# Kernel tuning notes

Measured on AMD Instinct MI355X. Metric: run time of the kernel, lower is better.

## Reference

```python
import jax, jax.numpy as jnp
import numpy as np

DIM = 1024
N_HEADS = 16
HEAD_DIM = DIM // N_HEADS
SCALE = HEAD_DIM ** (-0.5)


def setup_inputs() -> dict:
    key = jax.random.key(0)
    ks = jax.random.split(key, 5)
    B, N = 2, 1024
    x = jax.random.normal(ks[0], (B, N, DIM), dtype=jnp.float32)
    # torch nn.Linear convention: weight is (out_features, in_features)
    w_qkvg = jax.random.normal(ks[1], (4 * DIM, DIM), dtype=jnp.float32) * (DIM ** -0.5)
    b_qkvg = jax.random.normal(ks[2], (4 * DIM,), dtype=jnp.float32) * 0.02
    w_proj = jax.random.normal(ks[3], (DIM, DIM), dtype=jnp.float32) * (DIM ** -0.5)
    b_proj = jax.random.normal(ks[4], (DIM,), dtype=jnp.float32) * 0.02
    return {"x": x, "w_qkvg": w_qkvg, "b_qkvg": b_qkvg, "w_proj": w_proj, "b_proj": b_proj}


def reference(x, w_qkvg, b_qkvg, w_proj, b_proj):
    B, N, dim = x.shape
    # fused qkvg projection: (B, N, 4*dim)
    qkvg = x @ w_qkvg.T + b_qkvg
    # (B, N, 4, H, hd) -> (4, B, H, N, hd)
    qkvg = qkvg.reshape(B, N, 4, N_HEADS, HEAD_DIM).transpose(2, 0, 3, 1, 4)
    q = jax.nn.softplus(qkvg[0])          # (B, H, N, hd)
    k = jax.nn.softplus(qkvg[1])          # (B, H, N, hd)
    v = jax.nn.gelu(qkvg[2], approximate=False)  # (B, H, N, hd)
    g = jax.nn.gelu(qkvg[3], approximate=False)  # (B, H, N, hd)
    # kv = k @ v^T over head_dim -> (B, H, N, N)
    kv = jnp.einsum('bhnd,bhmd->bhnm', k, v)
    # z: contract q over tokens with per-token k-sums -> (B, H, hd)
    z = jnp.einsum('bhcn,bhc->bhn', q, k.sum(axis=-1)) * SCALE
    z = 1.0 / (z + dim)
    # out[b,h,d,n] = sum_c q[b,h,c,n] * kv[b,h,c,d] -> (B, H, N, hd)
    out = jnp.einsum('bhcn,bhcd->bhdn', q, kv) * SCALE
    out = (out + v) * z[:, :, None, :]    # broadcast z over token axis
    out = out.reshape(B, N, dim)          # raw reshape, faithful to original
    out = out * g.reshape(B, N, dim)
    out = out @ w_proj.T + b_proj
    return out
```

## Files before the change

kernel.cpp:

```cpp
#include <hip/hip_runtime.h>
#include <hip/hip_bf16.h>
#include <math.h>

typedef float f32x4 __attribute__((ext_vector_type(4)));
typedef __bf16 bf16_t;
typedef bf16_t bf16x8 __attribute__((ext_vector_type(8)));
typedef bf16_t bf16x4 __attribute__((ext_vector_type(4)));

__device__ __forceinline__ float act_softplus(float x) {
    return fmaxf(x, 0.f) + log1pf(expf(-fabsf(x)));
}
__device__ __forceinline__ float act_gelu(float x) {
    return 0.5f * x * (1.f + erff(x * 0.70710678118654752f));
}

__device__ __forceinline__ void gload_lds16(const bf16_t* g, bf16_t* l) {
    __builtin_amdgcn_global_load_lds(
        (const __attribute__((address_space(1))) unsigned int*)g,
        (__attribute__((address_space(3))) unsigned int*)l, 16, 0, 0);
}

template<int N_IMM>
__device__ __forceinline__ void wait_vmcnt() {
    if constexpr (N_IMM == 0) asm volatile("s_waitcnt vmcnt(0)" ::: "memory");
    else if constexpr (N_IMM == 2) asm volatile("s_waitcnt vmcnt(2)" ::: "memory");
    else if constexpr (N_IMM == 4) asm volatile("s_waitcnt vmcnt(4)" ::: "memory");
    else static_assert(N_IMM == 0, "unsupported vmcnt");
}

__global__ __launch_bounds__(256) void cvt3(const float* __restrict__ a, bf16_t* __restrict__ ao, int na4,
                                            const float* __restrict__ b, bf16_t* __restrict__ bo, int nb4,
                                            const float* __restrict__ c, bf16_t* __restrict__ co, int nc4) {
    int q = blockIdx.x * 256 + threadIdx.x;
    const float* src; bf16_t* dst;
    if (q < na4)            { src = a + (size_t)q * 4;              dst = ao + (size_t)q * 4; }
    else if (q < na4 + nb4) { int r = q - na4; src = b + (size_t)r * 4; dst = bo + (size_t)r * 4; }
    else if (q < na4 + nb4 + nc4) { int r = q - na4 - nb4; src = c + (size_t)r * 4; dst = co + (size_t)r * 4; }
    else return;
    float4 v = *reinterpret_cast<const float4*>(src);
    bf16x4 o;
    o[0] = (bf16_t)v.x; o[1] = (bf16_t)v.y; o[2] = (bf16_t)v.z; o[3] = (bf16_t)v.w;
    *reinterpret_cast<bf16x4*>(dst) = o;
}

__global__ __launch_bounds__(256) void gemm_qkvg(const bf16_t* __restrict__ A,
                                                 const bf16_t* __restrict__ Wall,
                                                 const float* __restrict__ biasAll,
                                                 bf16_t* __restrict__ OutAll) {
    constexpr int BM = 64, BN = 64, MR = 2, NR = 2;
    constexpr int K = 1024, M = 2048, N = 1024;
    constexpr int TNUM = K / 32;
    constexpr int LOADS = 2;

    __shared__ __align__(16) bf16_t Sa0[BM * 32];
    __shared__ __align__(16) bf16_t Sb0[BN * 32];
    __shared__ __align__(16) bf16_t Sa1[BM * 32];
    __shared__ __align__(16) bf16_t Sb1[BN * 32];

    const int sec = blockIdx.x >> 9;
    const int bid = blockIdx.x & 511;
    const bf16_t* B = Wall + (size_t)sec * 1024 * 1024;
    const float* bias = biasAll + sec * 1024;
    bf16_t* Cout = OutAll + (size_t)sec * 2048 * 1024;

    const int tid = threadIdx.x;
    const int lane = tid & 63;
    const int w = tid >> 6;
    const int wr = w >> 1, wc = w & 1;

    const int NTM = M / BM, NTN = N / BN;
    const int CHM = NTM >> 3;
    const int chunkN = (NTN * CHM) >> 3;
    const int c = bid & 7;
    const int pp = bid >> 3;
    const int mt = (c % CHM) * 8 + (pp & 7);
    const int nt = (c / CHM) * chunkN + (pp >> 3);
    const int m0 = mt * BM, n0 = nt * BN;

    const int l15 = lane & 15, lg = lane >> 4;
    const int srow = lane >> 2, pos = lane & 3;

    f32x4 acc[MR][NR] = {};

    auto stageTo = [&](bf16_t* Ad, bf16_t* Bd, int k0) {
        int row = w * 16 + srow;
        int ch = pos ^ ((row >> 1) & 3);
        gload_lds16(&A[(size_t)(m0 + row) * K + k0 + ch * 8], &Ad[w * 512]);
        gload_lds16(&B[(size_t)(n0 + row) * K + k0 + ch * 8], &Bd[w * 512]);
    };

    auto compute = [&](const bf16_t* Ac, const bf16_t* Bc) {
        bf16x8 af[MR], bfr[NR];
#pragma unroll
        for (int i = 0; i < MR; ++i) {
            int ar = wr * MR * 16 + i * 16 + l15;
            af[i] = *(const bf16x8*)(&Ac[ar * 32 + (lg ^ ((ar >> 1) & 3)) * 8]);
        }
#pragma unroll
        for (int j = 0; j < NR; ++j) {
            int br = wc * NR * 16 + j * 16 + l15;
            bfr[j] = *(const bf16x8*)(&Bc[br * 32 + (lg ^ ((br >> 1) & 3)) * 8]);
        }
#pragma unroll
        for (int i = 0; i < MR; ++i)
#pragma unroll
            for (int j = 0; j < NR; ++j)
                acc[i][j] = __builtin_amdgcn_mfma_f32_16x16x32_bf16(af[i], bfr[j], acc[i][j], 0, 0, 0);
    };

    stageTo(Sa0, Sb0, 0);
    for (int t = 0; t < TNUM; t += 2) {
        if (t + 1 < TNUM) { stageTo(Sa1, Sb1, (t + 1) * 32); wait_vmcnt<LOADS>(); }
        else              { wait_vmcnt<0>(); }
        __builtin_amdgcn_s_barrier();
        __builtin_amdgcn_sched_barrier(0);
        compute(Sa0, Sb0);
        __builtin_amdgcn_sched_barrier(0);
        __builtin_amdgcn_s_barrier();

        if (t + 2 < TNUM) { stageTo(Sa0, Sb0, (t + 2) * 32); wait_vmcnt<LOADS>(); }
        else              { wait_vmcnt<0>(); }
        __builtin_amdgcn_s_barrier();
        __builtin_amdgcn_sched_barrier(0);
        compute(Sa1, Sb1);
        __builtin_amdgcn_sched_barrier(0);
        __builtin_amdgcn_s_barrier();
    }

    bf16_t* slab = &Sb1[w * 512];
#pragma unroll
    for (int i = 0; i < MR; ++i) {
#pragma unroll
        for (int j = 0; j < NR; ++j) {
            int gn = n0 + wc * 32 + j * 16 + l15;
            float bv = bias[gn];
#pragma unroll
            for (int r = 0; r < 4; ++r) {
                float v = acc[i][j][r] + bv;
                float a = (sec < 2) ? act_softplus(v) : act_gelu(v);
                slab[(lg * 4 + r) * 32 + j * 16 + l15] = (bf16_t)a;
            }
        }
        int row = lane >> 2, c8 = (lane & 3) * 8;
        bf16x8 val = *(const bf16x8*)(&slab[row * 32 + c8]);
        *(bf16x8*)(&Cout[(size_t)(m0 + wr * 32 + i * 16 + row) * N + n0 + wc * 32 + c8]) = val;
        __builtin_amdgcn_s_barrier();
    }
}

template<int BM, int BN, int MR, int NR>
__global__ __launch_bounds__(256) void gemm_bt(const bf16_t* __restrict__ A,
                                               const bf16_t* __restrict__ B,
                                               const float* __restrict__ bias,
                                               float* __restrict__ Cout,
                                               int M, int N) {
    constexpr int K = 1024;
    constexpr int TNUM = K / 32;
    constexpr int WCOLS = BN / (NR * 16);
    constexpr int WROWS = BM / (MR * 16);
    static_assert(WROWS * WCOLS == 4, "4 waves");
    constexpr int ASEG = BM / 64, BSEG = BN / 64;
    constexpr int LOADS = ASEG + BSEG;

    __shared__ __align__(16) bf16_t Sa0[BM * 32];
    __shared__ __align__(16) bf16_t Sb0[BN * 32];
    __shared__ __align__(16) bf16_t Sa1[BM * 32];
    __shared__ __align__(16) bf16_t Sb1[BN * 32];
    __shared__ __align__(16) bf16_t Sa2[BM * 32];
    __shared__ __align__(16) bf16_t Sb2[BN * 32];

    const int tid = threadIdx.x;
    const int lane = tid & 63;
    const int w = tid >> 6;
    const int wr = w / WCOLS, wc = w % WCOLS;

    const int NTM = M / BM, NTN = N / BN;
    const int CHM = NTM >> 3;
    const int chunkN = (NTN * CHM) >> 3;
    const int c = blockIdx.x & 7;
    const int pp = blockIdx.x >> 3;
    const int mt = (c % CHM) * 8 + (pp & 7);
    const int nt = (c / CHM) * chunkN + (pp >> 3);
    const int m0 = mt * BM, n0 = nt * BN;

    const int l15 = lane & 15, lg = lane >> 4;
    const int srow = lane >> 2, pos = lane & 3;

    f32x4 acc[MR][NR] = {};

    auto stageTo = [&](bf16_t* Ad, bf16_t* Bd, int k0) {
#pragma unroll
        for (int t = 0; t < ASEG; ++t) {
            int s = w + t * 4;
            int row = s * 16 + srow;
            int ch = pos ^ ((row >> 1) & 3);
            gload_lds16(&A[(size_t)(m0 + row) * K + k0 + ch * 8], &Ad[s * 512]);
        }
#pragma unroll
        for (int t = 0; t < BSEG; ++t) {
            int s = w + t * 4;
            int row = s * 16 + srow;
            int ch = pos ^ ((row >> 1) & 3);
            gload_lds16(&B[(size_t)(n0 + row) * K + k0 + ch * 8], &Bd[s * 512]);
        }
    };

    auto compute = [&](const bf16_t* Ac, const bf16_t* Bc) {
        bf16x8 af[MR], bfr[NR];
#pragma unroll
        for (int i = 0; i < MR; ++i) {
            int ar = wr * MR * 16 + i * 16 + l15;
            af[i] = *(const bf16x8*)(&Ac[ar * 32 + (lg ^ ((ar >> 1) & 3)) * 8]);
        }
#pragma unroll
        for (int j = 0; j < NR; ++j) {
            int br = wc * NR * 16 + j * 16 + l15;
            bfr[j] = *(const bf16x8*)(&Bc[br * 32 + (lg ^ ((br >> 1) & 3)) * 8]);
        }
#pragma unroll
        for (int i = 0; i < MR; ++i)
#pragma unroll
            for (int j = 0; j < NR; ++j)
                acc[i][j] = __builtin_amdgcn_mfma_f32_16x16x32_bf16(af[i], bfr[j], acc[i][j], 0, 0, 0);
    };

    stageTo(Sa0, Sb0, 0);
    stageTo(Sa1, Sb1, 32);

    for (int t = 0; t < TNUM - 2; t += 3) {
        wait_vmcnt<LOADS>();
        __builtin_amdgcn_s_barrier();
        __builtin_amdgcn_sched_barrier(0);
        stageTo(Sa2, Sb2, (t + 2) * 32);
        compute(Sa0, Sb0);
        __builtin_amdgcn_sched_barrier(0);

        wait_vmcnt<LOADS>();
        __builtin_amdgcn_s_barrier();
        __builtin_amdgcn_sched_barrier(0);
        stageTo(Sa0, Sb0, (t + 3) * 32);
        compute(Sa1, Sb1);
        __builtin_amdgcn_sched_barrier(0);

        wait_vmcnt<LOADS>();
        __builtin_amdgcn_s_barrier();
        __builtin_amdgcn_sched_barrier(0);
        stageTo(Sa1, Sb1, (t + 4) * 32);
        compute(Sa2, Sb2);
        __builtin_amdgcn_sched_barrier(0);
    }
    wait_vmcnt<LOADS>();
    __builtin_amdgcn_s_barrier();
    __builtin_amdgcn_sched_barrier(0);
    compute(Sa0, Sb0);
    __builtin_amdgcn_sched_barrier(0);

    wait_vmcnt<0>();
    __builtin_amdgcn_s_barrier();
    __builtin_amdgcn_sched_barrier(0);
    compute(Sa1, Sb1);

#pragma unroll
    for (int i = 0; i < MR; ++i) {
        int gm_base = m0 + wr * MR * 16 + i * 16 + lg * 4;
#pragma unroll
        for (int j = 0; j < NR; ++j) {
            int gn = n0 + wc * NR * 16 + j * 16 + l15;
            float bv = bias[gn];
#pragma unroll
            for (int r = 0; r < 4; ++r) {
                int gm = gm_base + r;
                Cout[(size_t)gm * N + gn] = acc[i][j][r] + bv;
            }
        }
    }
}

__global__ __launch_bounds__(256) void attn_A(const bf16_t* __restrict__ qkvga,
                                              float* __restrict__ Apart) {
    const int bh = blockIdx.x;
    const int p = blockIdx.y;
    const int b = bh >> 4, h = bh & 15;
    const int tid = threadIdx.x;
    __shared__ float ks[32][64];
    __shared__ float qs[32][64];
    float acc[4][4] = {};
    const int dg = tid >> 4, eg = tid & 15;
    const int stok = tid >> 3, se0 = (tid & 7) * 8;
    const bf16_t* qf = qkvga;
    const bf16_t* kf = qkvga + (size_t)2048 * 1024;

    for (int t0 = p * 128; t0 < p * 128 + 128; t0 += 32) {
        __syncthreads();
        size_t rowb = (size_t)(b * 1024 + t0 + stok) * 1024 + h * 64 + se0;
        bf16x8 qv8 = *(const bf16x8*)(&qf[rowb]);
        bf16x8 kv8 = *(const bf16x8*)(&kf[rowb]);
#pragma unroll
        for (int jj = 0; jj < 8; ++jj) {
            qs[stok][se0 + jj] = (float)qv8[jj];
            ks[stok][se0 + jj] = (float)kv8[jj];
        }
        __syncthreads();
#pragma unroll 8
        for (int tt = 0; tt < 32; ++tt) {
            f32x4 kv = *(const f32x4*)(&ks[tt][dg * 4]);
            f32x4 qv = *(const f32x4*)(&qs[tt][eg * 4]);
#pragma unroll
            for (int i = 0; i < 4; ++i)
#pragma unroll
                for (int j = 0; j < 4; ++j) acc[i][j] += kv[i] * qv[j];
        }
    }
    float* dst = Apart + ((size_t)p * 32 + bh) * 4096;
#pragma unroll
    for (int i = 0; i < 4; ++i)
#pragma unroll
        for (int j = 0; j < 4; ++j)
            dst[(dg * 4 + i) * 64 + eg * 4 + j] = acc[i][j];
}

__global__ __launch_bounds__(256) void reduce_A_z(const float* __restrict__ Apart,
                                                  float* __restrict__ A,
                                                  float* __restrict__ z) {
    const int bh = blockIdx.x;
    const int tid = threadIdx.x;
    __shared__ float As[4096];
    for (int i0 = tid * 4; i0 < 4096; i0 += 1024) {
        f32x4 s = {};
#pragma unroll
        for (int p = 0; p < 8; ++p) {
            f32x4 v = *(const f32x4*)(&Apart[((size_t)p * 32 + bh) * 4096 + i0]);
            s += v;
        }
        *(f32x4*)(&As[i0]) = s;
        *(f32x4*)(&A[(size_t)bh * 4096 + i0]) = s;
    }
    __syncthreads();
    if (tid < 64) {
        float s = 0.f;
#pragma unroll 8
        for (int d = 0; d < 64; ++d) s += As[d * 64 + tid];
        z[bh * 64 + tid] = 1.0f / (s * 0.125f + 1024.0f);
    }
}

__global__ __launch_bounds__(256) void out_Y(const bf16_t* __restrict__ qkvga,
                                             const float* __restrict__ A,
                                             const float* __restrict__ z,
                                             bf16_t* __restrict__ Y) {
    const int bh = blockIdx.x;
    const int b = bh >> 4, h = bh & 15;
    const int chunk = blockIdx.y;
    const int tid = threadIdx.x;
    __shared__ float As[64][64];
    __shared__ float vs[32][64];
    __shared__ float zs[64];
    for (int i = tid; i < 4096; i += 256) As[i >> 6][i & 63] = A[(size_t)bh * 4096 + i];
    if (tid < 64) zs[tid] = z[bh * 64 + tid];
    const bf16_t* vf = qkvga + (size_t)2 * 2048 * 1024;
    const bf16_t* gf = qkvga + (size_t)3 * 2048 * 1024;
    const int e = tid & 63, trow = tid >> 6;
    const int stok = tid >> 3, se0 = (tid & 7) * 8;

    for (int t0 = chunk * 64; t0 < chunk * 64 + 64; t0 += 32) {
        __syncthreads();
        bf16x8 vv8 = *(const bf16x8*)(&vf[(size_t)(b * 1024 + t0 + stok) * 1024 + h * 64 + se0]);
#pragma unroll
        for (int jj = 0; jj < 8; ++jj) vs[stok][se0 + jj] = (float)vv8[jj];
        __syncthreads();
#pragma unroll
        for (int kk = 0; kk < 8; ++kk) {
            int ml = trow * 8 + kk;
            int m = t0 + ml;
            float s = 0.f;
#pragma unroll 8
            for (int d = 0; d < 64; ++d) s += vs[ml][d] * As[d][e];
            float g = (float)gf[(size_t)(b * 1024 + m) * 1024 + h * 64 + e];
            float o = (s * 0.125f + vs[ml][e]) * zs[e] * g;
            Y[((size_t)b * 1024 + h * 64 + (m >> 4)) * 1024 + ((m & 15) << 6) + e] = (bf16_t)o;
        }
    }
}

extern "C" void kernel_launch(void* const* d_in, const int* in_sizes, int n_in,
                              void* d_out, int out_size, void* d_ws, size_t ws_size,
                              hipStream_t stream) {
    const float* x      = (const float*)d_in[0];
    const float* w_qkvg = (const float*)d_in[1];
    const float* b_qkvg = (const float*)d_in[2];
    const float* w_proj = (const float*)d_in[3];
    const float* b_proj = (const float*)d_in[4];

    char* p = (char*)d_ws;
    bf16_t* xb    = (bf16_t*)p; p += (size_t)2048 * 1024 * 2;
    bf16_t* w1b   = (bf16_t*)p; p += (size_t)4096 * 1024 * 2;
    bf16_t* w2b   = (bf16_t*)p; p += (size_t)1024 * 1024 * 2;
    bf16_t* qkvga = (bf16_t*)p; p += (size_t)4 * 2048 * 1024 * 2;
    float*  Apart = (float*)p;  p += (size_t)8 * 32 * 4096 * 4;
    float*  Afull = (float*)p;  p += (size_t)32 * 4096 * 4;
    float*  zbuf  = (float*)p;  p += (size_t)32 * 64 * 4;
    bf16_t* Ybuf  = (bf16_t*)p; p += (size_t)2048 * 1024 * 2;

    cvt3<<<7168, 256, 0, stream>>>(x, xb, 524288, w_qkvg, w1b, 1048576, w_proj, w2b, 262144);

    gemm_qkvg<<<2048, 256, 0, stream>>>(xb, w1b, b_qkvg, qkvga);

    attn_A<<<dim3(32, 8), 256, 0, stream>>>(qkvga, Apart);
    reduce_A_z<<<32, 256, 0, stream>>>(Apart, Afull, zbuf);
    out_Y<<<dim3(32, 16), 256, 0, stream>>>(qkvga, Afull, zbuf, Ybuf);
    gemm_bt<64, 64, 2, 2><<<512, 256, 0, stream>>>(Ybuf, w2b, b_proj, (float*)d_out, 2048, 1024);
}
```

Baseline: 95.79 us.

## Rewrite QKVG projection GEMM with 256x256 tiles, 8 waves and triple buffering

```diff
diff --git a/kernel.cpp b/kernel.cpp
--- a/kernel.cpp
+++ b/kernel.cpp
@@ -43,108 +43,133 @@
     *reinterpret_cast<bf16x4*>(dst) = o;
 }
 
-__global__ __launch_bounds__(256) void gemm_qkvg(const bf16_t* __restrict__ A,
+__global__ __launch_bounds__(512) void gemm1_8ph(const bf16_t* __restrict__ Ag,
                                                  const bf16_t* __restrict__ Wall,
                                                  const float* __restrict__ biasAll,
                                                  bf16_t* __restrict__ OutAll) {
-    constexpr int BM = 64, BN = 64, MR = 2, NR = 2;
-    constexpr int K = 1024, M = 2048, N = 1024;
-    constexpr int TNUM = K / 32;
-    constexpr int LOADS = 2;
-
-    __shared__ __align__(16) bf16_t Sa0[BM * 32];
-    __shared__ __align__(16) bf16_t Sb0[BN * 32];
-    __shared__ __align__(16) bf16_t Sa1[BM * 32];
-    __shared__ __align__(16) bf16_t Sb1[BN * 32];
-
-    const int sec = blockIdx.x >> 9;
-    const int bid = blockIdx.x & 511;
-    const bf16_t* B = Wall + (size_t)sec * 1024 * 1024;
-    const float* bias = biasAll + sec * 1024;
-    bf16_t* Cout = OutAll + (size_t)sec * 2048 * 1024;
+    constexpr int K = 1024;
+    constexpr int NKT = K / 32;
+    __shared__ __align__(16) bf16_t SA0[256 * 32];
+    __shared__ __align__(16) bf16_t SA1[256 * 32];
+    __shared__ __align__(16) bf16_t SA2[256 * 32];
+    __shared__ __align__(16) bf16_t SB0[256 * 32];
+    __shared__ __align__(16) bf16_t SB1[256 * 32];
+    __shared__ __align__(16) bf16_t SB2[256 * 32];
 
     const int tid = threadIdx.x;
     const int lane = tid & 63;
     const int w = tid >> 6;
-    const int wr = w >> 1, wc = w & 1;
-
-    const int NTM = M / BM, NTN = N / BN;
-    const int CHM = NTM >> 3;
-    const int chunkN = (NTN * CHM) >> 3;
-    const int c = bid & 7;
-    const int pp = bid >> 3;
-    const int mt = (c % CHM) * 8 + (pp & 7);
-    const int nt = (c / CHM) * chunkN + (pp >> 3);
-    const int m0 = mt * BM, n0 = nt * BN;
+    const int wr = w >> 2, wc = w & 3;
+
+    const int c = blockIdx.x & 7;
+    const int pp = blockIdx.x >> 3;
+    const int mt = pp & 7;
+    const int nt = c * 2 + (pp >> 3);
+    const int m0 = mt * 256;
+    const int sec = nt >> 2;
+    const int nc0 = (nt & 3) * 256;
+    const bf16_t* Bg = Wall + (size_t)sec * 1024 * 1024;
+    const float* bias = biasAll + sec * 1024;
+    bf16_t* Cout = OutAll + (size_t)sec * 2048 * 1024;
 
     const int l15 = lane & 15, lg = lane >> 4;
     const int srow = lane >> 2, pos = lane & 3;
 
-    f32x4 acc[MR][NR] = {};
-
-    auto stageTo = [&](bf16_t* Ad, bf16_t* Bd, int k0) {
-        int row = w * 16 + srow;
+    f32x4 acc[2][2][4][2] = {};
+
+    auto stageA = [&](bf16_t* Ad, int kg, int s) {
+        int row = s * 128 + w * 16 + srow;
         int ch = pos ^ ((row >> 1) & 3);
-        gload_lds16(&A[(size_t)(m0 + row) * K + k0 + ch * 8], &Ad[w * 512]);
-        gload_lds16(&B[(size_t)(n0 + row) * K + k0 + ch * 8], &Bd[w * 512]);
+        gload_lds16(&Ag[(size_t)(m0 + row) * K + kg + ch * 8], Ad + (s * 128 + w * 16) * 32);
     };
-
-    auto compute = [&](const bf16_t* Ac, const bf16_t* Bc) {
-        bf16x8 af[MR], bfr[NR];
-#pragma unroll
-        for (int i = 0; i < MR; ++i) {
-            int ar = wr * MR * 16 + i * 16 + l15;
-            af[i] = *(const bf16x8*)(&Ac[ar * 32 + (lg ^ ((ar >> 1) & 3)) * 8]);
-        }
-#pragma unroll
-        for (int j = 0; j < NR; ++j) {
-            int br = wc * NR * 16 + j * 16 + l15;
-            bfr[j] = *(const bf16x8*)(&Bc[br * 32 + (lg ^ ((br >> 1) & 3)) * 8]);
-        }
-#pragma unroll
-        for (int i = 0; i < MR; ++i)
-#pragma unroll
-            for (int j = 0; j < NR; ++j)
-                acc[i][j] = __builtin_amdgcn_mfma_f32_16x16x32_bf16(af[i], bfr[j], acc[i][j], 0, 0, 0);
+    auto stageB = [&](bf16_t* Bd, int kg, int s) {
+        int row = s * 128 + w * 16 + srow;
+        int ch = pos ^ ((row >> 1) & 3);
+        gload_lds16(&Bg[(size_t)(nc0 + row) * K + kg + ch * 8], Bd + (s * 128 + w * 16) * 32);
     };
 
-    stageTo(Sa0, Sb0, 0);
-    for (int t = 0; t < TNUM; t += 2) {
-        if (t + 1 < TNUM) { stageTo(Sa1, Sb1, (t + 1) * 32); wait_vmcnt<LOADS>(); }
-        else              { wait_vmcnt<0>(); }
-        __builtin_amdgcn_s_barrier();
-        __builtin_amdgcn_sched_barrier(0);
-        compute(Sa0, Sb0);
-        __builtin_amdgcn_sched_barrier(0);
-        __builtin_amdgcn_s_barrier();
-
-        if (t + 2 < TNUM) { stageTo(Sa0, Sb0, (t + 2) * 32); wait_vmcnt<LOADS>(); }
-        else              { wait_vmcnt<0>(); }
-        __builtin_amdgcn_s_barrier();
-        __builtin_amdgcn_sched_barrier(0);
-        compute(Sa1, Sb1);
-        __builtin_amdgcn_sched_barrier(0);
-        __builtin_amdgcn_s_barrier();
-    }
-
-    bf16_t* slab = &Sb1[w * 512];
-#pragma unroll
-    for (int i = 0; i < MR; ++i) {
-#pragma unroll
-        for (int j = 0; j < NR; ++j) {
-            int gn = n0 + wc * 32 + j * 16 + l15;
-            float bv = bias[gn];
-#pragma unroll
-            for (int r = 0; r < 4; ++r) {
-                float v = acc[i][j][r] + bv;
-                float a = (sec < 2) ? act_softplus(v) : act_gelu(v);
-                slab[(lg * 4 + r) * 32 + j * 16 + l15] = (bf16_t)a;
+    stageA(SA0, 0, 0);  stageA(SA0, 0, 1);  stageB(SB0, 0, 0);  stageB(SB0, 0, 1);
+    stageA(SA1, 32, 0); stageA(SA1, 32, 1); stageB(SB1, 32, 0); stageB(SB1, 32, 1);
+    wait_vmcnt<4>();
+    __builtin_amdgcn_s_barrier();
+    __builtin_amdgcn_sched_barrier(0);
+
+    int cur = 0;
+    for (int kt = 0; kt < NKT; ++kt) {
+        const bf16_t* Ac = (cur == 0) ? SA0 : (cur == 1) ? SA1 : SA2;
+        const bf16_t* Bc = (cur == 0) ? SB0 : (cur == 1) ? SB1 : SB2;
+        int stg = (cur == 0) ? 2 : cur - 1;
+        bf16_t* Ast = (stg == 0) ? SA0 : (stg == 1) ? SA1 : SA2;
+        bf16_t* Bst = (stg == 0) ? SB0 : (stg == 1) ? SB1 : SB2;
+        const bool doStage = (kt + 2 < NKT);
+        const int kg = (kt + 2) * 32;
+
+#pragma unroll
+        for (int q = 0; q < 4; ++q) {
+            const int qr = q >> 1, qc = q & 1;
+            bf16x8 af[4], bfv[2];
+#pragma unroll
+            for (int fi = 0; fi < 4; ++fi) {
+                int r = wr * 128 + qr * 64 + fi * 16 + l15;
+                af[fi] = *(const bf16x8*)(&Ac[r * 32 + (lg ^ ((r >> 1) & 3)) * 8]);
             }
-        }
-        int row = lane >> 2, c8 = (lane & 3) * 8;
-        bf16x8 val = *(const bf16x8*)(&slab[row * 32 + c8]);
-        *(bf16x8*)(&Cout[(size_t)(m0 + wr * 32 + i * 16 + row) * N + n0 + wc * 32 + c8]) = val;
-        __builtin_amdgcn_s_barrier();
+#pragma unroll
+            for (int fj = 0; fj < 2; ++fj) {
+                int cc = wc * 64 + qc * 32 + fj * 16 + l15;
+                bfv[fj] = *(const bf16x8*)(&Bc[cc * 32 + (lg ^ ((cc >> 1) & 3)) * 8]);
+            }
+            if (doStage) {
+                if (q == 0)      stageA(Ast, kg, 0);
+                else if (q == 1) stageA(Ast, kg, 1);
+                else if (q == 2) stageB(Bst, kg, 0);
+                else             stageB(Bst, kg, 1);
+            }
+            if (q == 3) {
+                if (kt == NKT - 2)      wait_vmcnt<0>();
+                else if (kt < NKT - 2)  wait_vmcnt<4>();
+            }
+            __builtin_amdgcn_s_barrier();
+            __builtin_amdgcn_sched_barrier(0);
+            __builtin_amdgcn_s_setprio(1);
+#pragma unroll
+            for (int fi = 0; fi < 4; ++fi)
+#pragma unroll
+                for (int fj = 0; fj < 2; ++fj)
+                    acc[qr][qc][fi][fj] = __builtin_amdgcn_mfma_f32_16x16x32_bf16(
+                        af[fi], bfv[fj], acc[qr][qc][fi][fj], 0, 0, 0);
+            __builtin_amdgcn_s_setprio(0);
+            __builtin_amdgcn_sched_barrier(0);
+            __builtin_amdgcn_s_barrier();
+        }
+        cur = (cur == 2) ? 0 : cur + 1;
+    }
+
+    bf16_t* slab = SA0 + w * 1024;
+    const int colbase = nc0 + wc * 64;
+#pragma unroll
+    for (int qr = 0; qr < 2; ++qr) {
+#pragma unroll
+        for (int fi = 0; fi < 4; ++fi) {
+#pragma unroll
+            for (int qc = 0; qc < 2; ++qc)
+#pragma unroll
+                for (int fj = 0; fj < 2; ++fj) {
+                    int col = colbase + qc * 32 + fj * 16 + l15;
+                    float bv = bias[col];
+#pragma unroll
+                    for (int rr = 0; rr < 4; ++rr) {
+                        float v = acc[qr][qc][fi][fj][rr] + bv;
+                        float a = (sec < 2) ? act_softplus(v) : act_gelu(v);
+                        slab[(lg * 4 + rr) * 64 + qc * 32 + fj * 16 + l15] = (bf16_t)a;
+                    }
+                }
+            int row16 = lane >> 2, seg = (lane & 3) * 8;
+            int gr = m0 + wr * 128 + qr * 64 + fi * 16 + row16;
+            bf16x8 v0 = *(const bf16x8*)(&slab[row16 * 64 + seg]);
+            bf16x8 v1 = *(const bf16x8*)(&slab[row16 * 64 + 32 + seg]);
+            *(bf16x8*)(&Cout[(size_t)gr * 1024 + colbase + seg]) = v0;
+            *(bf16x8*)(&Cout[(size_t)gr * 1024 + colbase + 32 + seg]) = v1;
+        }
     }
 }
 
@@ -403,7 +428,7 @@
 
     cvt3<<<7168, 256, 0, stream>>>(x, xb, 524288, w_qkvg, w1b, 1048576, w_proj, w2b, 262144);
 
-    gemm_qkvg<<<2048, 256, 0, stream>>>(xb, w1b, b_qkvg, qkvga);
+    gemm1_8ph<<<128, 512, 0, stream>>>(xb, w1b, b_qkvg, qkvga);
 
     attn_A<<<dim3(32, 8), 256, 0, stream>>>(qkvga, Apart);
     reduce_A_z<<<32, 256, 0, stream>>>(Apart, Afull, zbuf);
```

Result: slower. 282.4 us (+194.8%).

## Triple-buffer QKVG GEMM and split-K output projection across two wave quads

Applied to the files above, without the earlier changes.

```diff
diff --git a/kernel.cpp b/kernel.cpp
--- a/kernel.cpp
+++ b/kernel.cpp
@@ -56,6 +56,8 @@
     __shared__ __align__(16) bf16_t Sb0[BN * 32];
     __shared__ __align__(16) bf16_t Sa1[BM * 32];
     __shared__ __align__(16) bf16_t Sb1[BN * 32];
+    __shared__ __align__(16) bf16_t Sa2[BM * 32];
+    __shared__ __align__(16) bf16_t Sb2[BN * 32];
 
     const int sec = blockIdx.x >> 9;
     const int bid = blockIdx.x & 511;
@@ -82,7 +84,7 @@
 
     f32x4 acc[MR][NR] = {};
 
-    auto stageTo = [&](bf16_t* Ad, bf16_t* Bd, int k0) {
+    auto stageTo2 = [&](bf16_t* Ad, bf16_t* Bd, int k0) {
         int row = w * 16 + srow;
         int ch = pos ^ ((row >> 1) & 3);
         gload_lds16(&A[(size_t)(m0 + row) * K + k0 + ch * 8], &Ad[w * 512]);
@@ -108,26 +110,43 @@
                 acc[i][j] = __builtin_amdgcn_mfma_f32_16x16x32_bf16(af[i], bfr[j], acc[i][j], 0, 0, 0);
     };
 
-    stageTo(Sa0, Sb0, 0);
-    for (int t = 0; t < TNUM; t += 2) {
-        if (t + 1 < TNUM) { stageTo(Sa1, Sb1, (t + 1) * 32); wait_vmcnt<LOADS>(); }
-        else              { wait_vmcnt<0>(); }
-        __builtin_amdgcn_s_barrier();
-        __builtin_amdgcn_sched_barrier(0);
+    stageTo2(Sa0, Sb0, 0);
+    stageTo2(Sa1, Sb1, 32);
+
+    for (int t = 0; t < TNUM - 2; t += 3) {
+        wait_vmcnt<LOADS>();
+        __builtin_amdgcn_s_barrier();
+        __builtin_amdgcn_sched_barrier(0);
+        stageTo2(Sa2, Sb2, (t + 2) * 32);
         compute(Sa0, Sb0);
         __builtin_amdgcn_sched_barrier(0);
-        __builtin_amdgcn_s_barrier();
-
-        if (t + 2 < TNUM) { stageTo(Sa0, Sb0, (t + 2) * 32); wait_vmcnt<LOADS>(); }
-        else              { wait_vmcnt<0>(); }
-        __builtin_amdgcn_s_barrier();
-        __builtin_amdgcn_sched_barrier(0);
+
+        wait_vmcnt<LOADS>();
+        __builtin_amdgcn_s_barrier();
+        __builtin_amdgcn_sched_barrier(0);
+        stageTo2(Sa0, Sb0, (t + 3) * 32);
         compute(Sa1, Sb1);
         __builtin_amdgcn_sched_barrier(0);
-        __builtin_amdgcn_s_barrier();
-    }
-
-    bf16_t* slab = &Sb1[w * 512];
+
+        wait_vmcnt<LOADS>();
+        __builtin_amdgcn_s_barrier();
+        __builtin_amdgcn_sched_barrier(0);
+        stageTo2(Sa1, Sb1, (t + 4) * 32);
+        compute(Sa2, Sb2);
+        __builtin_amdgcn_sched_barrier(0);
+    }
+    wait_vmcnt<LOADS>();
+    __builtin_amdgcn_s_barrier();
+    __builtin_amdgcn_sched_barrier(0);
+    compute(Sa0, Sb0);
+    __builtin_amdgcn_sched_barrier(0);
+
+    wait_vmcnt<0>();
+    __builtin_amdgcn_s_barrier();
+    __builtin_amdgcn_sched_barrier(0);
+    compute(Sa1, Sb1);
+
+    bf16_t* slab = &Sb2[w * 512];
 #pragma unroll
     for (int i = 0; i < MR; ++i) {
 #pragma unroll
@@ -144,133 +163,111 @@
         int row = lane >> 2, c8 = (lane & 3) * 8;
         bf16x8 val = *(const bf16x8*)(&slab[row * 32 + c8]);
         *(bf16x8*)(&Cout[(size_t)(m0 + wr * 32 + i * 16 + row) * N + n0 + wc * 32 + c8]) = val;
-        __builtin_amdgcn_s_barrier();
-    }
-}
-
-template<int BM, int BN, int MR, int NR>
-__global__ __launch_bounds__(256) void gemm_bt(const bf16_t* __restrict__ A,
-                                               const bf16_t* __restrict__ B,
-                                               const float* __restrict__ bias,
-                                               float* __restrict__ Cout,
-                                               int M, int N) {
-    constexpr int K = 1024;
-    constexpr int TNUM = K / 32;
-    constexpr int WCOLS = BN / (NR * 16);
-    constexpr int WROWS = BM / (MR * 16);
-    static_assert(WROWS * WCOLS == 4, "4 waves");
-    constexpr int ASEG = BM / 64, BSEG = BN / 64;
-    constexpr int LOADS = ASEG + BSEG;
-
-    __shared__ __align__(16) bf16_t Sa0[BM * 32];
-    __shared__ __align__(16) bf16_t Sb0[BN * 32];
-    __shared__ __align__(16) bf16_t Sa1[BM * 32];
-    __shared__ __align__(16) bf16_t Sb1[BN * 32];
-    __shared__ __align__(16) bf16_t Sa2[BM * 32];
-    __shared__ __align__(16) bf16_t Sb2[BN * 32];
+    }
+}
+
+__global__ __launch_bounds__(512) void gemm2_sk(const bf16_t* __restrict__ A,
+                                                const bf16_t* __restrict__ B,
+                                                const float* __restrict__ bias,
+                                                float* __restrict__ Cout) {
+    constexpr int M = 2048, N = 1024, K = 1024;
+    constexpr int TNUM = 16;
+    __shared__ __align__(16) bf16_t Sa[2][2][64 * 32];
+    __shared__ __align__(16) bf16_t Sb[2][2][64 * 32];
+    __shared__ float red[64 * 64];
 
     const int tid = threadIdx.x;
     const int lane = tid & 63;
     const int w = tid >> 6;
-    const int wr = w / WCOLS, wc = w % WCOLS;
-
-    const int NTM = M / BM, NTN = N / BN;
+    const int quad = w >> 2;
+    const int wq = w & 3;
+    const int wr = wq >> 1, wc = wq & 1;
+
+    const int NTM = M / 64, NTN = N / 64;
     const int CHM = NTM >> 3;
     const int chunkN = (NTN * CHM) >> 3;
     const int c = blockIdx.x & 7;
     const int pp = blockIdx.x >> 3;
     const int mt = (c % CHM) * 8 + (pp & 7);
     const int nt = (c / CHM) * chunkN + (pp >> 3);
-    const int m0 = mt * BM, n0 = nt * BN;
+    const int m0 = mt * 64, n0 = nt * 64;
 
     const int l15 = lane & 15, lg = lane >> 4;
     const int srow = lane >> 2, pos = lane & 3;
-
-    f32x4 acc[MR][NR] = {};
+    const int kbase = quad * 512;
+
+    f32x4 acc[2][2] = {};
+    bf16_t* SaQ0 = Sa[quad][0]; bf16_t* SbQ0 = Sb[quad][0];
+    bf16_t* SaQ1 = Sa[quad][1]; bf16_t* SbQ1 = Sb[quad][1];
 
     auto stageTo = [&](bf16_t* Ad, bf16_t* Bd, int k0) {
-#pragma unroll
-        for (int t = 0; t < ASEG; ++t) {
-            int s = w + t * 4;
-            int row = s * 16 + srow;
-            int ch = pos ^ ((row >> 1) & 3);
-            gload_lds16(&A[(size_t)(m0 + row) * K + k0 + ch * 8], &Ad[s * 512]);
-        }
-#pragma unroll
-        for (int t = 0; t < BSEG; ++t) {
-            int s = w + t * 4;
-            int row = s * 16 + srow;
-            int ch = pos ^ ((row >> 1) & 3);
-            gload_lds16(&B[(size_t)(n0 + row) * K + k0 + ch * 8], &Bd[s * 512]);
-        }
+        int row = wq * 16 + srow;
+        int ch = pos ^ ((row >> 1) & 3);
+        gload_lds16(&A[(size_t)(m0 + row) * K + kbase + k0 + ch * 8], &Ad[wq * 512]);
+        gload_lds16(&B[(size_t)(n0 + row) * K + kbase + k0 + ch * 8], &Bd[wq * 512]);
     };
 
     auto compute = [&](const bf16_t* Ac, const bf16_t* Bc) {
-        bf16x8 af[MR], bfr[NR];
-#pragma unroll
-        for (int i = 0; i < MR; ++i) {
-            int ar = wr * MR * 16 + i * 16 + l15;
+        bf16x8 af[2], bfr[2];
+#pragma unroll
+        for (int i = 0; i < 2; ++i) {
+            int ar = wr * 32 + i * 16 + l15;
             af[i] = *(const bf16x8*)(&Ac[ar * 32 + (lg ^ ((ar >> 1) & 3)) * 8]);
         }
 #pragma unroll
-        for (int j = 0; j < NR; ++j) {
-            int br = wc * NR * 16 + j * 16 + l15;
+        for (int j = 0; j < 2; ++j) {
+            int br = wc * 32 + j * 16 + l15;
             bfr[j] = *(const bf16x8*)(&Bc[br * 32 + (lg ^ ((br >> 1) & 3)) * 8]);
         }
 #pragma unroll
-        for (int i = 0; i < MR; ++i)
-#pragma unroll
-            for (int j = 0; j < NR; ++j)
+        for (int i = 0; i < 2; ++i)
+#pragma unroll
+            for (int j = 0; j < 2; ++j)
                 acc[i][j] = __builtin_amdgcn_mfma_f32_16x16x32_bf16(af[i], bfr[j], acc[i][j], 0, 0, 0);
     };
 
-    stageTo(Sa0, Sb0, 0);
-    stageTo(Sa1, Sb1, 32);
-
-    for (int t = 0; t < TNUM - 2; t += 3) {
-        wait_vmcnt<LOADS>();
-        __builtin_amdgcn_s_barrier();
-        __builtin_amdgcn_sched_barrier(0);
-        stageTo(Sa2, Sb2, (t + 2) * 32);
-        compute(Sa0, Sb0);
-        __builtin_amdgcn_sched_barrier(0);
-
-        wait_vmcnt<LOADS>();
-        __builtin_amdgcn_s_barrier();
-        __builtin_amdgcn_sched_barrier(0);
-        stageTo(Sa0, Sb0, (t + 3) * 32);
-        compute(Sa1, Sb1);
-        __builtin_amdgcn_sched_barrier(0);
-
-        wait_vmcnt<LOADS>();
-        __builtin_amdgcn_s_barrier();
-        __builtin_amdgcn_sched_barrier(0);
-        stageTo(Sa1, Sb1, (t + 4) * 32);
-        compute(Sa2, Sb2);
-        __builtin_amdgcn_sched_barrier(0);
-    }
-    wait_vmcnt<LOADS>();
-    __builtin_amdgcn_s_barrier();
-    __builtin_amdgcn_sched_barrier(0);
-    compute(Sa0, Sb0);
-    __builtin_amdgcn_sched_barrier(0);
-
-    wait_vmcnt<0>();
-    __builtin_amdgcn_s_barrier();
-    __builtin_amdgcn_sched_barrier(0);
-    compute(Sa1, Sb1);
-
-#pragma unroll
-    for (int i = 0; i < MR; ++i) {
-        int gm_base = m0 + wr * MR * 16 + i * 16 + lg * 4;
-#pragma unroll
-        for (int j = 0; j < NR; ++j) {
-            int gn = n0 + wc * NR * 16 + j * 16 + l15;
-            float bv = bias[gn];
-#pragma unroll
-            for (int r = 0; r < 4; ++r) {
-                int gm = gm_base + r;
-                Cout[(size_t)gm * N + gn] = acc[i][j][r] + bv;
+    stageTo(SaQ0, SbQ0, 0);
+    for (int t = 0; t < TNUM; t += 2) {
+        if (t + 1 < TNUM) { stageTo(SaQ1, SbQ1, (t + 1) * 32); wait_vmcnt<2>(); }
+        else              { wait_vmcnt<0>(); }
+        __builtin_amdgcn_s_barrier();
+        __builtin_amdgcn_sched_barrier(0);
+        compute(SaQ0, SbQ0);
+        __builtin_amdgcn_sched_barrier(0);
+        __builtin_amdgcn_s_barrier();
+
+        if (t + 2 < TNUM) { stageTo(SaQ0, SbQ0, (t + 2) * 32); wait_vmcnt<2>(); }
+        else              { wait_vmcnt<0>(); }
+        __builtin_amdgcn_s_barrier();
+        __builtin_amdgcn_sched_barrier(0);
+        compute(SaQ1, SbQ1);
+        __builtin_amdgcn_sched_barrier(0);
+        __builtin_amdgcn_s_barrier();
+    }
+
+    if (quad == 1) {
+#pragma unroll
+        for (int i = 0; i < 2; ++i)
+#pragma unroll
+            for (int j = 0; j < 2; ++j)
+#pragma unroll
+                for (int r = 0; r < 4; ++r)
+                    red[(wr * 32 + i * 16 + lg * 4 + r) * 64 + wc * 32 + j * 16 + l15] = acc[i][j][r];
+    }
+    __syncthreads();
+    if (quad == 0) {
+#pragma unroll
+        for (int i = 0; i < 2; ++i) {
+#pragma unroll
+            for (int j = 0; j < 2; ++j) {
+                int lcol = wc * 32 + j * 16 + l15;
+                int gn = n0 + lcol;
+                float bv = bias[gn];
+#pragma unroll
+                for (int r = 0; r < 4; ++r) {
+                    int lrow = wr * 32 + i * 16 + lg * 4 + r;
+                    Cout[(size_t)(m0 + lrow) * N + gn] = acc[i][j][r] + red[lrow * 64 + lcol] + bv;
+                }
             }
         }
     }
@@ -408,5 +405,5 @@
     attn_A<<<dim3(32, 8), 256, 0, stream>>>(qkvga, Apart);
     reduce_A_z<<<32, 256, 0, stream>>>(Apart, Afull, zbuf);
     out_Y<<<dim3(32, 16), 256, 0, stream>>>(qkvga, Afull, zbuf, Ybuf);
-    gemm_bt<64, 64, 2, 2><<<512, 256, 0, stream>>>(Ybuf, w2b, b_proj, (float*)d_out, 2048, 1024);
-}
+    gemm2_sk<<<512, 512, 0, stream>>>(Ybuf, w2b, b_proj, (float*)d_out);
+}
```

After: 95.16 us. About the same (-0.7%).
